# Kernel tuning notes

Hardware: AMD Instinct MI355X
Metric: run time of the kernel (lower is better)

## Reference

```python
import jax, jax.numpy as jnp
import numpy as np

N = 30000   # nodes
E = 600000  # edges (avg degree 20)
H = 128     # hidden_channels
L = 4       # num_layers
G = 64      # graphs in batch


def _init(key, shape, fan_in):
    return (jax.random.normal(key, shape, jnp.float32) / np.sqrt(fan_in)).astype(jnp.float32)


def setup_inputs() -> dict:
    key = jax.random.key(0)
    ks = jax.random.split(key, 24)
    x = jax.random.normal(ks[0], (N, 1), jnp.float32)
    pos = jax.random.normal(ks[1], (N, 3), jnp.float32)
    edge_index = jax.random.randint(ks[2], (2, E), 0, N, dtype=jnp.int32).astype(jnp.int64)
    batch = jnp.sort(jax.random.randint(ks[3], (N,), 0, G, dtype=jnp.int32)).astype(jnp.int64)

    emb_w = _init(ks[4], (1, H), 1)
    emb_b = jnp.zeros((H,), jnp.float32)

    # stacked per-layer params: msg MLP (2H+1 -> H -> H), node MLP (2H -> H -> H)
    msg_w1 = _init(ks[5], (L, 2 * H + 1, H), 2 * H + 1)
    msg_b1 = jnp.zeros((L, H), jnp.float32)
    msg_w2 = _init(ks[6], (L, H, H), H)
    msg_b2 = jnp.zeros((L, H), jnp.float32)
    node_w1 = _init(ks[7], (L, 2 * H, H), 2 * H)
    node_b1 = jnp.zeros((L, H), jnp.float32)
    node_w2 = _init(ks[8], (L, H, H), H)
    node_b2 = jnp.zeros((L, H), jnp.float32)

    out_w1 = _init(ks[9], (H, 32), H)
    out_b1 = jnp.zeros((32,), jnp.float32)
    out_w2 = _init(ks[10], (32, 1), 32)
    out_b2 = jnp.zeros((1,), jnp.float32)

    return {
        "x": x, "pos": pos, "edge_index": edge_index, "batch": batch,
        "emb_w": emb_w, "emb_b": emb_b,
        "msg_w1": msg_w1, "msg_b1": msg_b1, "msg_w2": msg_w2, "msg_b2": msg_b2,
        "node_w1": node_w1, "node_b1": node_b1, "node_w2": node_w2, "node_b2": node_b2,
        "out_w1": out_w1, "out_b1": out_b1, "out_w2": out_w2, "out_b2": out_b2,
    }


def reference(x, pos, edge_index, batch,
              emb_w, emb_b,
              msg_w1, msg_b1, msg_w2, msg_b2,
              node_w1, node_b1, node_w2, node_b2,
              out_w1, out_b1, out_w2, out_b2):
    row, col = edge_index[0], edge_index[1]  # row = source j, col = target i
    # edge scalar: squared distance (computed once, reused across layers)
    dist_sq = jnp.sum((pos[row] - pos[col]) ** 2, axis=-1, keepdims=True)  # [E,1]

    h = x @ emb_w + emb_b  # [N,H]
    for l in range(L):
        x_j = h[row]   # source features
        x_i = h[col]   # target features
        m = jnp.concatenate([x_i, x_j, dist_sq], axis=-1)           # [E, 2H+1]
        m = jax.nn.silu(m @ msg_w1[l] + msg_b1[l]) @ msg_w2[l] + msg_b2[l]  # [E,H]
        aggr = jax.ops.segment_sum(m, col, num_segments=N)          # scatter-add to targets
        nh = jnp.concatenate([h, aggr], axis=-1)                    # [N, 2H]
        h = jax.nn.silu(nh @ node_w1[l] + node_b1[l]) @ node_w2[l] + node_b2[l]
        # dropout omitted for deterministic reference (eval mode)

    g = jax.ops.segment_sum(h, batch, num_segments=G)               # global_add_pool [G,H]
    return jax.nn.silu(g @ out_w1 + out_b1) @ out_w2 + out_b2       # [G,1]
```

## Files before the change

### kernel.cpp

```cpp
#include <hip/hip_runtime.h>

typedef unsigned short u16;
typedef __bf16 bf16x8 __attribute__((ext_vector_type(8)));
typedef float f32x4 __attribute__((ext_vector_type(4)));

#define HN 128
#define TM 64
#define ASTRIDE 136

__device__ __forceinline__ u16 f2bf(float f) {
  union { float f; unsigned u; } v; v.f = f;
  unsigned r = v.u + 0x7fffu + ((v.u >> 16) & 1u);
  return (u16)(r >> 16);
}
__device__ __forceinline__ float bf2f(u16 v) {
  union { unsigned u; float f; } x; x.u = ((unsigned)v) << 16; return x.f;
}
__device__ __forceinline__ float bflo(unsigned v) {
  union { unsigned u; float f; } x; x.u = v << 16; return x.f;
}
__device__ __forceinline__ float bfhi(unsigned v) {
  union { unsigned u; float f; } x; x.u = v & 0xffff0000u; return x.f;
}
__device__ __forceinline__ float silu_f(float x) {
  float e = __builtin_amdgcn_exp2f(-1.442695041f * x);
  return x * __builtin_amdgcn_rcpf(1.f + e);
}

__global__ void pack_weights(const float* __restrict__ msg_w1, const float* __restrict__ msg_w2,
                             const float* __restrict__ node_w1, const float* __restrict__ node_w2,
                             u16* __restrict__ pw, int* __restrict__ deg,
                             float* __restrict__ g, int N_, int GH) {
  int id = blockIdx.x * 256 + threadIdx.x;
  if (id < N_) deg[id] = 0;
  if (id < GH) g[id] = 0.f;
  if (id >= 4 * 6 * 16384) return;
  int l = id / (6 * 16384);
  int rem = id % (6 * 16384);
  int m = rem / 16384;
  int e = rem % 16384;
  int kg = e >> 10;
  int n = (e >> 3) & 127;
  int j = e & 7;
  int k = kg * 8 + j;
  float v = 0.f;
  switch (m) {
    case 0: v = msg_w1[(l * 257 + k) * 128 + n]; break;
    case 1: v = msg_w1[(l * 257 + 128 + k) * 128 + n]; break;
    case 2: v = msg_w2[(l * 128 + k) * 128 + n]; break;
    case 3: v = node_w1[(l * 256 + k) * 128 + n]; break;
    case 4: v = node_w1[(l * 256 + 128 + k) * 128 + n]; break;
    case 5: v = node_w2[(l * 128 + k) * 128 + n]; break;
  }
  pw[id] = f2bf(v);
}

__device__ __forceinline__ void gemm64(const u16* s_A, const u16* s_W,
                                       int w, int quad, int m16, f32x4 acc[8]) {
#pragma unroll
  for (int ks = 0; ks < 4; ks++) {
    bf16x8 a = *(const bf16x8*)&s_A[(w * 16 + m16) * ASTRIDE + ks * 32 + quad * 8];
#pragma unroll
    for (int ct = 0; ct < 8; ct++) {
      bf16x8 b = *(const bf16x8*)&s_W[(ks * 4 + quad) * 1024 + (ct * 16 + m16) * 8];
      acc[ct] = __builtin_amdgcn_mfma_f32_16x16x32_bf16(a, b, acc[ct], 0, 0, 0);
    }
  }
}

__device__ __forceinline__ void gemm64_gb(const u16* s_A, const u16* __restrict__ gW,
                                          int w, int quad, int m16, f32x4 acc[8]) {
#pragma unroll
  for (int ks = 0; ks < 4; ks++) {
    bf16x8 a = *(const bf16x8*)&s_A[(w * 16 + m16) * ASTRIDE + ks * 32 + quad * 8];
#pragma unroll
    for (int ct = 0; ct < 8; ct++) {
      bf16x8 b = *(const bf16x8*)&gW[(ks * 4 + quad) * 1024 + (ct * 16 + m16) * 8];
      acc[ct] = __builtin_amdgcn_mfma_f32_16x16x32_bf16(a, b, acc[ct], 0, 0, 0);
    }
  }
}

__device__ __forceinline__ void gemm64_ra_gb(const bf16x8 aH[4], const u16* __restrict__ gW,
                                             int quad, int m16, f32x4 acc[8]) {
#pragma unroll
  for (int ks = 0; ks < 4; ks++) {
#pragma unroll
    for (int ct = 0; ct < 8; ct++) {
      bf16x8 b = *(const bf16x8*)&gW[(ks * 4 + quad) * 1024 + (ct * 16 + m16) * 8];
      acc[ct] = __builtin_amdgcn_mfma_f32_16x16x32_bf16(aH[ks], b, acc[ct], 0, 0, 0);
    }
  }
}

__global__ __launch_bounds__(256) void fold_kernel(
    const float* __restrict__ msg_w2, const float* __restrict__ node_w1,
    const float* __restrict__ msg_b2, const u16* __restrict__ pw,
    u16* __restrict__ pwc, float* __restrict__ vc) {
  __shared__ __align__(16) u16 s_A[TM * ASTRIDE];
  __shared__ __align__(16) u16 s_W[16384];
  const int t = threadIdx.x;
  const int w = t >> 6, lane = t & 63, quad = lane >> 4, m16 = lane & 15;
  const int b = blockIdx.x, l = b >> 1, half = b & 1;
  const int tile0 = half * 64;

  {
    int r = t >> 2, qo = (t & 3) * 32;
    const float4* src = (const float4*)(msg_w2 + (size_t)(l * 128 + tile0 + r) * 128 + qo);
    u16* dst = s_A + r * ASTRIDE + qo;
#pragma unroll
    for (int i = 0; i < 8; i++) {
      float4 v = src[i];
      ushort4 o;
      o.x = f2bf(v.x); o.y = f2bf(v.y); o.z = f2bf(v.z); o.w = f2bf(v.w);
      *(ushort4*)(dst + i * 4) = o;
    }
  }
  {
    const int4* src = (const int4*)(pw + (size_t)(l * 6 + 4) * 16384);
    int4* dst = (int4*)s_W;
#pragma unroll
    for (int i = 0; i < 8; i++) dst[t + i * 256] = src[t + i * 256];
  }
  __syncthreads();
  f32x4 acc[8];
#pragma unroll
  for (int ct = 0; ct < 8; ct++) acc[ct] = {0.f, 0.f, 0.f, 0.f};
  gemm64(s_A, s_W, w, quad, m16, acc);
#pragma unroll
  for (int ct = 0; ct < 8; ct++)
#pragma unroll
    for (int j = 0; j < 4; j++) {
      int k = tile0 + w * 16 + quad * 4 + j;
      int n = ct * 16 + m16;
      pwc[(size_t)l * 16384 + (k >> 3) * 1024 + n * 8 + (k & 7)] = f2bf(acc[ct][j]);
    }
  if (half == 0 && t < 128) {
    float s = 0.f;
    for (int np = 0; np < 128; np++)
      s += msg_b2[l * 128 + np] * node_w1[(size_t)(l * 256 + 128 + np) * 128 + t];
    vc[l * 128 + t] = s;
  }
}

__global__ void hist_kernel(const int* __restrict__ eidx, int* __restrict__ deg,
                            int* __restrict__ rnk, int E_) {
  int e = blockIdx.x * 256 + threadIdx.x;
  if (e < E_) rnk[e] = atomicAdd(&deg[eidx[E_ + e]], 1);
}

__global__ void scan1_kernel(const int* __restrict__ deg, int* __restrict__ off,
                             int* __restrict__ bsum, int n) {
  __shared__ int s[256];
  int t = threadIdx.x;
  int i = blockIdx.x * 256 + t;
  int v = (i < n) ? deg[i] : 0;
  s[t] = v;
  for (int d = 1; d < 256; d <<= 1) {
    __syncthreads();
    int x = (t >= d) ? s[t - d] : 0;
    __syncthreads();
    s[t] += x;
  }
  __syncthreads();
  if (i < n) off[i] = s[t] - v;
  if (t == 255) bsum[blockIdx.x] = s[255];
}

__global__ void scan2_kernel(int* __restrict__ bsum, int nb) {
  __shared__ int s[256];
  int t = threadIdx.x;
  int v = (t < nb) ? bsum[t] : 0;
  s[t] = v;
  for (int d = 1; d < 256; d <<= 1) {
    __syncthreads();
    int x = (t >= d) ? s[t - d] : 0;
    __syncthreads();
    s[t] += x;
  }
  __syncthreads();
  if (t < nb) bsum[t] = s[t] - v;
}

__global__ void scan3_kernel(int* __restrict__ off, const int* __restrict__ bsum, int n) {
  int i = blockIdx.x * 256 + threadIdx.x;
  if (i < n) off[i] += bsum[blockIdx.x];
}

__global__ void scatter_kernel(const int* __restrict__ eidx, const float* __restrict__ pos,
                               const int* __restrict__ off, const int* __restrict__ rnk,
                               int2* __restrict__ es8, int E_) {
  int e = blockIdx.x * 256 + threadIdx.x;
  if (e >= E_) return;
  int sr = eidx[e], tg = eidx[E_ + e];
  float dx = pos[sr * 3 + 0] - pos[tg * 3 + 0];
  float dy = pos[sr * 3 + 1] - pos[tg * 3 + 1];
  float dz = pos[sr * 3 + 2] - pos[tg * 3 + 2];
  float d = dx * dx + dy * dy + dz * dz;
  int p = off[tg] + rnk[e];
  int2 v;
  v.x = sr | (tg << 15);
  v.y = __float_as_int(d);
  es8[p] = v;
}

__global__ __launch_bounds__(256) void proj_kernel(
    const float* __restrict__ x, const float* __restrict__ emb_w,
    const float* __restrict__ emb_b, u16* __restrict__ hbf,
    u16* __restrict__ Pout, u16* __restrict__ Qout,
    const u16* __restrict__ pw, const float* __restrict__ b1, int nnodes) {
  const int t = threadIdx.x;
  const int w = t >> 6, lane = t & 63, quad = lane >> 4, m16 = lane & 15;
  const int tile0 = blockIdx.x * TM;

  int nodem = tile0 + w * 16 + m16;
  bool live = nodem < nnodes;
  if (!live) nodem = nnodes - 1;
  float xv = x[nodem];
  bf16x8 aH[4];
#pragma unroll
  for (int ks = 0; ks < 4; ks++) {
    u16 hv[8];
#pragma unroll
    for (int i = 0; i < 8; i++) {
      int c = ks * 32 + quad * 8 + i;
      hv[i] = f2bf(xv * emb_w[c] + emb_b[c]);
    }
    aH[ks] = *(bf16x8*)hv;
    if (live) *(int4*)&hbf[(size_t)nodem * HN + ks * 32 + quad * 8] = *(int4*)hv;
  }
  float bb[8];
#pragma unroll
  for (int ct = 0; ct < 8; ct++) bb[ct] = b1[ct * 16 + m16];

  f32x4 acc[8];
#pragma unroll
  for (int ct = 0; ct < 8; ct++) acc[ct] = {0.f, 0.f, 0.f, 0.f};
  gemm64_ra_gb(aH, pw, quad, m16, acc);
#pragma unroll
  for (int ct = 0; ct < 8; ct++)
#pragma unroll
    for (int j = 0; j < 4; j++) {
      int n = tile0 + w * 16 + quad * 4 + j;
      if (n < nnodes) Pout[(size_t)n * HN + ct * 16 + m16] = f2bf(acc[ct][j] + bb[ct]);
    }
#pragma unroll
  for (int ct = 0; ct < 8; ct++) acc[ct] = {0.f, 0.f, 0.f, 0.f};
  gemm64_ra_gb(aH, pw + 16384, quad, m16, acc);
#pragma unroll
  for (int ct = 0; ct < 8; ct++)
#pragma unroll
    for (int j = 0; j < 4; j++) {
      int n = tile0 + w * 16 + quad * 4 + j;
      if (n < nnodes) Qout[(size_t)n * HN + ct * 16 + m16] = f2bf(acc[ct][j]);
    }
}

__device__ __forceinline__ void edge_step_lds(
    int tg_s, float dd_s, unsigned qv,
    int& cur_s, float& p0, float& p1, float& s0, float& s1,
    const u16* __restrict__ P, float* s_S, int cp,
    float wd0, float wd1, int tile0) {
  if (tg_s != cur_s) {
    if (cur_s >= 0) {
      float* dst = &s_S[(cur_s - tile0) * HN + cp];
      atomicAdd(dst, s0);
      atomicAdd(dst + 1, s1);
    }
    cur_s = tg_s; s0 = 0.f; s1 = 0.f;
    int cg = tg_s < 0 ? 0 : tg_s;
    unsigned pv = *(const unsigned*)&P[(size_t)cg * HN + cp];
    p0 = bflo(pv); p1 = bfhi(pv);
  }
  float x0 = p0 + bflo(qv) + dd_s * wd0;
  float x1 = p1 + bfhi(qv) + dd_s * wd1;
  s0 += silu_f(x0);
  s1 += silu_f(x1);
}

template <bool FUSE>
__global__ __launch_bounds__(256) void layer_kernel(
    const u16* __restrict__ P, const u16* __restrict__ Q,
    const u16* __restrict__ hbf, u16* __restrict__ hout,
    const int* __restrict__ off, const int* __restrict__ deg,
    const float* __restrict__ w1d, const int2* __restrict__ es8,
    const u16* __restrict__ pwc, const float* __restrict__ vc,
    const u16* __restrict__ pwn, const float* __restrict__ b1, const float* __restrict__ b2,
    const u16* __restrict__ pw_next, const float* __restrict__ b1_next,
    u16* __restrict__ Pout, u16* __restrict__ Qout, int nnodes, int E_) {
  __shared__ float s_S[TM * HN];
  __shared__ __align__(16) u16 s_A[TM * ASTRIDE];
  const int t = threadIdx.x;
  const int w = t >> 6, lane = t & 63, quad = lane >> 4, m16 = lane & 15;
  const int tile0 = blockIdx.x * TM;
  u16* band = s_A + (w * 16) * ASTRIDE;

  {
    float4 z = {0.f, 0.f, 0.f, 0.f};
    float4* p4 = (float4*)s_S;
#pragma unroll
    for (int i = 0; i < 8; i++) p4[t + i * 256] = z;
  }
  __syncthreads();

  const int cp = lane * 2;
  const float2 wdv = *(const float2*)&w1d[cp];
  const float wd0 = wdv.x, wd1 = wdv.y;
  const int e_lo = off[tile0];
  const int e_hi = (tile0 + TM < nnodes) ? off[tile0 + TM] : E_;
  const int span = e_hi - e_lo;
  const int wstart = e_lo + (span * w) / 4;
  const int wend = e_lo + (span * (w + 1)) / 4;
  const int total = wend - wstart;
  const int nchunks = (total + 63) >> 6;

  int cur_s = -1;
  float s0 = 0.f, s1 = 0.f, p0 = 0.f, p1 = 0.f;

  if (nchunks > 0) {
    int2* ebuf = (int2*)band;
    {
      int e = wstart + lane;
      int2 v;
      if (e < wend) v = es8[e];
      else { v.x = (int)0xFFFF8000; v.y = 0; }
      ebuf[lane] = v;
    }
    asm volatile("s_waitcnt lgkmcnt(0)" ::: "memory");
    int tg[8]; float dd[8]; unsigned qv[8];
#pragma unroll
    for (int j = 0; j < 8; j++) {
      int2 v = ebuf[j];
      tg[j] = v.x >> 15; dd[j] = __int_as_float(v.y);
      qv[j] = *(const unsigned*)&Q[(size_t)(v.x & 0x7fff) * HN + cp];
    }

    for (int ci = 0; ci < nchunks; ci++) {
      const int2* cb = ebuf + (ci & 1) * 64;
      const int2* nb = ebuf + ((ci + 1) & 1) * 64;
      int2 vnext; vnext.x = (int)0xFFFF8000; vnext.y = 0;
      {
        int e = wstart + (ci + 1) * 64 + lane;
        if (ci + 1 < nchunks && e < wend) vnext = es8[e];
      }
#pragma unroll
      for (int g = 0; g < 7; g++) {
        int tgn[8]; float ddn[8]; unsigned qvn[8];
#pragma unroll
        for (int j = 0; j < 8; j++) {
          int2 v = cb[(g + 1) * 8 + j];
          tgn[j] = v.x >> 15; ddn[j] = __int_as_float(v.y);
          qvn[j] = *(const unsigned*)&Q[(size_t)(v.x & 0x7fff) * HN + cp];
        }
#pragma unroll
        for (int j = 0; j < 8; j++) {
          int tg_s = __builtin_amdgcn_readfirstlane(tg[j]);
          edge_step_lds(tg_s, dd[j], qv[j], cur_s, p0, p1, s0, s1, P, s_S, cp, wd0, wd1, tile0);
        }
#pragma unroll
        for (int j = 0; j < 8; j++) { tg[j] = tgn[j]; dd[j] = ddn[j]; qv[j] = qvn[j]; }
      }
      ebuf[((ci + 1) & 1) * 64 + lane] = vnext;
      asm volatile("s_waitcnt lgkmcnt(0)" ::: "memory");
      {
        int tgn[8]; float ddn[8]; unsigned qvn[8];
#pragma unroll
        for (int j = 0; j < 8; j++) {
          int2 v = nb[j];
          tgn[j] = v.x >> 15; ddn[j] = __int_as_float(v.y);
          qvn[j] = *(const unsigned*)&Q[(size_t)(v.x & 0x7fff) * HN + cp];
        }
#pragma unroll
        for (int j = 0; j < 8; j++) {
          int tg_s = __builtin_amdgcn_readfirstlane(tg[j]);
          edge_step_lds(tg_s, dd[j], qv[j], cur_s, p0, p1, s0, s1, P, s_S, cp, wd0, wd1, tile0);
        }
#pragma unroll
        for (int j = 0; j < 8; j++) { tg[j] = tgn[j]; dd[j] = ddn[j]; qv[j] = qvn[j]; }
      }
    }
    if (cur_s >= 0) {
      float* dst = &s_S[(cur_s - tile0) * HN + cp];
      atomicAdd(dst, s0);
      atomicAdd(dst + 1, s1);
    }
  }
  __syncthreads();

  const int rb = lane >> 2;
  const int qo = (lane & 3) * 32;
  int nodem = tile0 + w * 16 + m16;
  if (nodem >= nnodes) nodem = nnodes - 1;

  float bb1[8], vcr[8], bb2[8], bbn[8];
#pragma unroll
  for (int ct = 0; ct < 8; ct++) {
    bb1[ct] = b1[ct * 16 + m16];
    vcr[ct] = vc[ct * 16 + m16];
    bb2[ct] = b2[ct * 16 + m16];
    bbn[ct] = FUSE ? b1_next[ct * 16 + m16] : 0.f;
  }

  {
    const float4* src = (const float4*)&s_S[(w * 16 + rb) * HN + qo];
    u16* dst = band + rb * ASTRIDE + qo;
#pragma unroll
    for (int i = 0; i < 8; i++) {
      float4 v = src[i];
      ushort4 o;
      o.x = f2bf(v.x); o.y = f2bf(v.y); o.z = f2bf(v.z); o.w = f2bf(v.w);
      *(ushort4*)(dst + i * 4) = o;
    }
  }
  asm volatile("s_waitcnt lgkmcnt(0)" ::: "memory");
  __builtin_amdgcn_sched_barrier(0);

  f32x4 acc[8];
#pragma unroll
  for (int ct = 0; ct < 8; ct++) acc[ct] = {0.f, 0.f, 0.f, 0.f};
  gemm64_gb(s_A, pwc, w, quad, m16, acc);

  bf16x8 aH[4];
#pragma unroll
  for (int ks = 0; ks < 4; ks++)
    aH[ks] = *(const bf16x8*)&hbf[(size_t)nodem * HN + ks * 32 + quad * 8];
  gemm64_ra_gb(aH, pwn, quad, m16, acc);

  {
    float degv[4];
#pragma unroll
    for (int j = 0; j < 4; j++) {
      int n = tile0 + w * 16 + quad * 4 + j;
      if (n >= nnodes) n = nnodes - 1;
      degv[j] = (float)deg[n];
    }
#pragma unroll
    for (int ct = 0; ct < 8; ct++)
#pragma unroll
      for (int j = 0; j < 4; j++) {
        int row = quad * 4 + j;
        float xv = acc[ct][j] + bb1[ct] + degv[j] * vcr[ct];
        band[row * ASTRIDE + ct * 16 + m16] = f2bf(silu_f(xv));
      }
  }
  asm volatile("s_waitcnt lgkmcnt(0)" ::: "memory");
  __builtin_amdgcn_sched_barrier(0);

#pragma unroll
  for (int ct = 0; ct < 8; ct++) acc[ct] = {0.f, 0.f, 0.f, 0.f};
  gemm64_gb(s_A, pwn + 32768, w, quad, m16, acc);

#pragma unroll
  for (int ct = 0; ct < 8; ct++)
#pragma unroll
    for (int j = 0; j < 4; j++) {
      int row = quad * 4 + j;
      int n = tile0 + w * 16 + row;
      u16 hv = f2bf(acc[ct][j] + bb2[ct]);
      if (n < nnodes) hout[(size_t)n * HN + ct * 16 + m16] = hv;
      if (FUSE) band[row * ASTRIDE + ct * 16 + m16] = hv;
    }

  if (FUSE) {
    asm volatile("s_waitcnt lgkmcnt(0)" ::: "memory");
    __builtin_amdgcn_sched_barrier(0);
#pragma unroll
    for (int ct = 0; ct < 8; ct++) acc[ct] = {0.f, 0.f, 0.f, 0.f};
    gemm64_gb(s_A, pw_next, w, quad, m16, acc);
#pragma unroll
    for (int ct = 0; ct < 8; ct++)
#pragma unroll
      for (int j = 0; j < 4; j++) {
        int n = tile0 + w * 16 + quad * 4 + j;
        if (n < nnodes) Pout[(size_t)n * HN + ct * 16 + m16] = f2bf(acc[ct][j] + bbn[ct]);
      }
#pragma unroll
    for (int ct = 0; ct < 8; ct++) acc[ct] = {0.f, 0.f, 0.f, 0.f};
    gemm64_gb(s_A, pw_next + 16384, w, quad, m16, acc);
#pragma unroll
    for (int ct = 0; ct < 8; ct++)
#pragma unroll
      for (int j = 0; j < 4; j++) {
        int n = tile0 + w * 16 + quad * 4 + j;
        if (n < nnodes) Qout[(size_t)n * HN + ct * 16 + m16] = f2bf(acc[ct][j]);
      }
  }
}

__global__ __launch_bounds__(256) void pool_kernel(
    const u16* __restrict__ h, const int* __restrict__ batch,
    float* __restrict__ g, int N) {
  __shared__ int s_b[64];
  const int t = threadIdx.x;
  const int n0 = blockIdx.x * 64;
  if (t < 64) {
    int n = n0 + t;
    s_b[t] = (n < N) ? batch[n] : -1;
  }
  __syncthreads();
  const int cp = (t & 63) * 2;
  const int rg = t >> 6;
  int cur = -1;
  float s0 = 0.f, s1 = 0.f;
#pragma unroll 4
  for (int i = 0; i < 16; i++) {
    int r = rg * 16 + i;
    int b = s_b[r];
    if (b < 0) break;
    if (b != cur) {
      if (cur >= 0) {
        atomicAdd(&g[cur * HN + cp], s0);
        atomicAdd(&g[cur * HN + cp + 1], s1);
      }
      cur = b; s0 = 0.f; s1 = 0.f;
    }
    unsigned v = *(const unsigned*)&h[(size_t)(n0 + r) * HN + cp];
    s0 += bf2f((u16)(v & 0xffffu));
    s1 += bf2f((u16)(v >> 16));
  }
  if (cur >= 0) {
    atomicAdd(&g[cur * HN + cp], s0);
    atomicAdd(&g[cur * HN + cp + 1], s1);
  }
}

__global__ __launch_bounds__(64) void out_kernel(
    const float* __restrict__ g, const float* __restrict__ w1,
    const float* __restrict__ b1, const float* __restrict__ w2,
    const float* __restrict__ b2, float* __restrict__ out) {
  const int gi = blockIdx.x;
  const int t = threadIdx.x;
  const int c = t & 31, kh = t >> 5;
  float s = 0.f;
  for (int k = kh * 64; k < kh * 64 + 64; k++)
    s += g[gi * HN + k] * w1[k * 32 + c];
  s += __shfl_down(s, 32);
  float r = 0.f;
  if (kh == 0) r = silu_f(s + b1[c]) * w2[c];
  r += __shfl_down(r, 16);
  r += __shfl_down(r, 8);
  r += __shfl_down(r, 4);
  r += __shfl_down(r, 2);
  r += __shfl_down(r, 1);
  if (t == 0) out[gi] = r + b2[0];
}

extern "C" void kernel_launch(void* const* d_in, const int* in_sizes, int n_in,
                              void* d_out, int out_size, void* d_ws, size_t ws_size,
                              hipStream_t stream) {
  const float* x = (const float*)d_in[0];
  const float* pos = (const float*)d_in[1];
  const int* eidx = (const int*)d_in[2];
  const int* batch = (const int*)d_in[3];
  const float* emb_w = (const float*)d_in[4];
  const float* emb_b = (const float*)d_in[5];
  const float* msg_w1 = (const float*)d_in[6];
  const float* msg_b1 = (const float*)d_in[7];
  const float* msg_w2 = (const float*)d_in[8];
  const float* msg_b2 = (const float*)d_in[9];
  const float* node_w1 = (const float*)d_in[10];
  const float* node_b1 = (const float*)d_in[11];
  const float* node_w2 = (const float*)d_in[12];
  const float* node_b2 = (const float*)d_in[13];
  const float* out_w1 = (const float*)d_in[14];
  const float* out_b1 = (const float*)d_in[15];
  const float* out_w2 = (const float*)d_in[16];
  const float* out_b2 = (const float*)d_in[17];
  float* outp = (float*)d_out;

  const int N = 30000, E = 600000, G = 64;
  const size_t NH = (size_t)N * HN;

  u16* hA = (u16*)d_ws;
  u16* hB = hA + NH;
  u16* Pa = hB + NH;
  u16* Qa = Pa + NH;
  u16* Pb = Qa + NH;
  u16* Qb = Pb + NH;
  int2* es8 = (int2*)(Qb + NH);
  int* deg = (int*)(es8 + E);
  int* off = deg + N;
  int* bsum = off + N;
  float* g = (float*)(bsum + 128);
  u16* pw = (u16*)(g + G * HN);
  u16* pwc = pw + (size_t)4 * 6 * 16384;
  float* vcb = (float*)(pwc + (size_t)4 * 16384);
  int* rnk = (int*)Pb;

  const int NB = (N + 255) / 256;
  const int NTB = (N + TM - 1) / TM;

  pack_weights<<<(4 * 6 * 16384 + 255) / 256, 256, 0, stream>>>(
      msg_w1, msg_w2, node_w1, node_w2, pw, deg, g, N, G * HN);
  fold_kernel<<<8, 256, 0, stream>>>(msg_w2, node_w1, msg_b2, pw, pwc, vcb);

  hist_kernel<<<(E + 255) / 256, 256, 0, stream>>>(eidx, deg, rnk, E);
  scan1_kernel<<<NB, 256, 0, stream>>>(deg, off, bsum, N);
  scan2_kernel<<<1, 256, 0, stream>>>(bsum, NB);
  scan3_kernel<<<NB, 256, 0, stream>>>(off, bsum, N);
  scatter_kernel<<<(E + 255) / 256, 256, 0, stream>>>(eidx, pos, off, rnk, es8, E);

  proj_kernel<<<NTB, 256, 0, stream>>>(x, emb_w, emb_b, hA, Pa, Qa, pw, msg_b1, N);

  u16* hcur = hA;
  u16* hnext = hB;
  u16* Pin = Pa; u16* Qin = Qa;
  u16* Pot = Pb; u16* Qot = Qb;
  for (int l = 0; l < 4; l++) {
    const u16* pwl = pw + (size_t)(l * 6) * 16384;
    const float* w1d = msg_w1 + (size_t)(l * 257 + 256) * 128;
    if (l < 3) {
      const u16* pw_next = pw + (size_t)((l + 1) * 6) * 16384;
      layer_kernel<true><<<NTB, 256, 0, stream>>>(
          Pin, Qin, hcur, hnext, off, deg, w1d, es8,
          pwc + (size_t)l * 16384, vcb + l * 128,
          pwl + 3 * 16384, node_b1 + l * 128, node_b2 + l * 128,
          pw_next, msg_b1 + (l + 1) * 128, Pot, Qot, N, E);
    } else {
      layer_kernel<false><<<NTB, 256, 0, stream>>>(
          Pin, Qin, hcur, hnext, off, deg, w1d, es8,
          pwc + (size_t)l * 16384, vcb + l * 128,
          pwl + 3 * 16384, node_b1 + l * 128, node_b2 + l * 128,
          nullptr, nullptr, nullptr, nullptr, N, E);
    }
    u16* tmp = hcur; hcur = hnext; hnext = tmp;
    tmp = Pin; Pin = Pot; Pot = tmp;
    tmp = Qin; Qin = Qot; Qot = tmp;
  }

  pool_kernel<<<(N + 63) / 64, 256, 0, stream>>>(hcur, batch, g, N);
  out_kernel<<<G, 64, 0, stream>>>(g, out_w1, out_b1, out_w2, out_b2, outp);
}
```

Baseline: 435.2 us.

## Halve layer node tile to 32 rows and stage projection weights in LDS

Result: faster. 399.4 us (-8.2%).

```diff
diff --git a/kernel.cpp b/kernel.cpp
--- a/kernel.cpp
+++ b/kernel.cpp
@@ -6,6 +6,7 @@
 
 #define HN 128
 #define TM 64
+#define LTM 32
 #define ASTRIDE 136
 
 __device__ __forceinline__ u16 f2bf(float f) {
@@ -68,26 +69,26 @@
   }
 }
 
-__device__ __forceinline__ void gemm64_gb(const u16* s_A, const u16* __restrict__ gW,
-                                          int w, int quad, int m16, f32x4 acc[8]) {
+__device__ __forceinline__ void gemm32_gb(const u16* s_A, const u16* __restrict__ gW,
+                                          int rh, int ch, int quad, int m16, f32x4 acc[4]) {
 #pragma unroll
   for (int ks = 0; ks < 4; ks++) {
-    bf16x8 a = *(const bf16x8*)&s_A[(w * 16 + m16) * ASTRIDE + ks * 32 + quad * 8];
-#pragma unroll
-    for (int ct = 0; ct < 8; ct++) {
-      bf16x8 b = *(const bf16x8*)&gW[(ks * 4 + quad) * 1024 + (ct * 16 + m16) * 8];
+    bf16x8 a = *(const bf16x8*)&s_A[(rh * 16 + m16) * ASTRIDE + ks * 32 + quad * 8];
+#pragma unroll
+    for (int ct = 0; ct < 4; ct++) {
+      bf16x8 b = *(const bf16x8*)&gW[(ks * 4 + quad) * 1024 + ((ch * 4 + ct) * 16 + m16) * 8];
       acc[ct] = __builtin_amdgcn_mfma_f32_16x16x32_bf16(a, b, acc[ct], 0, 0, 0);
     }
   }
 }
 
-__device__ __forceinline__ void gemm64_ra_gb(const bf16x8 aH[4], const u16* __restrict__ gW,
-                                             int quad, int m16, f32x4 acc[8]) {
+__device__ __forceinline__ void gemm32_ra_gb(const bf16x8 aH[4], const u16* __restrict__ gW,
+                                             int ch, int quad, int m16, f32x4 acc[4]) {
 #pragma unroll
   for (int ks = 0; ks < 4; ks++) {
 #pragma unroll
-    for (int ct = 0; ct < 8; ct++) {
-      bf16x8 b = *(const bf16x8*)&gW[(ks * 4 + quad) * 1024 + (ct * 16 + m16) * 8];
+    for (int ct = 0; ct < 4; ct++) {
+      bf16x8 b = *(const bf16x8*)&gW[(ks * 4 + quad) * 1024 + ((ch * 4 + ct) * 16 + m16) * 8];
       acc[ct] = __builtin_amdgcn_mfma_f32_16x16x32_bf16(aH[ks], b, acc[ct], 0, 0, 0);
     }
   }
@@ -209,34 +210,47 @@
     const float* __restrict__ emb_b, u16* __restrict__ hbf,
     u16* __restrict__ Pout, u16* __restrict__ Qout,
     const u16* __restrict__ pw, const float* __restrict__ b1, int nnodes) {
+  __shared__ __align__(16) u16 s_A[TM * ASTRIDE];
+  __shared__ __align__(16) u16 s_W[16384];
   const int t = threadIdx.x;
   const int w = t >> 6, lane = t & 63, quad = lane >> 4, m16 = lane & 15;
   const int tile0 = blockIdx.x * TM;
-
-  int nodem = tile0 + w * 16 + m16;
-  bool live = nodem < nnodes;
-  if (!live) nodem = nnodes - 1;
-  float xv = x[nodem];
-  bf16x8 aH[4];
-#pragma unroll
-  for (int ks = 0; ks < 4; ks++) {
-    u16 hv[8];
-#pragma unroll
-    for (int i = 0; i < 8; i++) {
-      int c = ks * 32 + quad * 8 + i;
-      hv[i] = f2bf(xv * emb_w[c] + emb_b[c]);
-    }
-    aH[ks] = *(bf16x8*)hv;
-    if (live) *(int4*)&hbf[(size_t)nodem * HN + ks * 32 + quad * 8] = *(int4*)hv;
+  {
+    int r = t >> 2, qo = (t & 3) * 32;
+    int node = tile0 + r;
+    if (node >= nnodes) node = nnodes - 1;
+    float xv = x[node];
+    u16 hv[32];
+#pragma unroll
+    for (int i = 0; i < 32; i++) hv[i] = f2bf(xv * emb_w[qo + i] + emb_b[qo + i]);
+    u16* dst = s_A + r * ASTRIDE + qo;
+#pragma unroll
+    for (int i = 0; i < 4; i++) *(int4*)(dst + i * 8) = *(int4*)(hv + i * 8);
+    u16* gd = hbf + (size_t)node * HN + qo;
+#pragma unroll
+    for (int i = 0; i < 4; i++) *(int4*)(gd + i * 8) = *(int4*)(hv + i * 8);
+  }
+  {
+    const int4* src = (const int4*)pw;
+    int4* dst = (int4*)s_W;
+#pragma unroll
+    for (int i = 0; i < 8; i++) dst[t + i * 256] = src[t + i * 256];
+  }
+  __syncthreads();
+  f32x4 acc[8];
+#pragma unroll
+  for (int ct = 0; ct < 8; ct++) acc[ct] = {0.f, 0.f, 0.f, 0.f};
+  gemm64(s_A, s_W, w, quad, m16, acc);
+  __syncthreads();
+  {
+    const int4* src = (const int4*)(pw + 16384);
+    int4* dst = (int4*)s_W;
+#pragma unroll
+    for (int i = 0; i < 8; i++) dst[t + i * 256] = src[t + i * 256];
   }
   float bb[8];
 #pragma unroll
   for (int ct = 0; ct < 8; ct++) bb[ct] = b1[ct * 16 + m16];
-
-  f32x4 acc[8];
-#pragma unroll
-  for (int ct = 0; ct < 8; ct++) acc[ct] = {0.f, 0.f, 0.f, 0.f};
-  gemm64_ra_gb(aH, pw, quad, m16, acc);
 #pragma unroll
   for (int ct = 0; ct < 8; ct++)
 #pragma unroll
@@ -244,9 +258,10 @@
       int n = tile0 + w * 16 + quad * 4 + j;
       if (n < nnodes) Pout[(size_t)n * HN + ct * 16 + m16] = f2bf(acc[ct][j] + bb[ct]);
     }
+  __syncthreads();
 #pragma unroll
   for (int ct = 0; ct < 8; ct++) acc[ct] = {0.f, 0.f, 0.f, 0.f};
-  gemm64_ra_gb(aH, pw + 16384, quad, m16, acc);
+  gemm64(s_A, s_W, w, quad, m16, acc);
 #pragma unroll
   for (int ct = 0; ct < 8; ct++)
 #pragma unroll
@@ -288,18 +303,19 @@
     const u16* __restrict__ pwn, const float* __restrict__ b1, const float* __restrict__ b2,
     const u16* __restrict__ pw_next, const float* __restrict__ b1_next,
     u16* __restrict__ Pout, u16* __restrict__ Qout, int nnodes, int E_) {
-  __shared__ float s_S[TM * HN];
-  __shared__ __align__(16) u16 s_A[TM * ASTRIDE];
+  __shared__ float s_S[LTM * HN];
+  __shared__ __align__(16) u16 s_A[LTM * ASTRIDE];
   const int t = threadIdx.x;
   const int w = t >> 6, lane = t & 63, quad = lane >> 4, m16 = lane & 15;
-  const int tile0 = blockIdx.x * TM;
-  u16* band = s_A + (w * 16) * ASTRIDE;
+  const int tile0 = blockIdx.x * LTM;
+  const int rh = w >> 1;
+  const int ch = w & 1;
 
   {
     float4 z = {0.f, 0.f, 0.f, 0.f};
     float4* p4 = (float4*)s_S;
 #pragma unroll
-    for (int i = 0; i < 8; i++) p4[t + i * 256] = z;
+    for (int i = 0; i < 4; i++) p4[t + i * 256] = z;
   }
   __syncthreads();
 
@@ -307,7 +323,7 @@
   const float2 wdv = *(const float2*)&w1d[cp];
   const float wd0 = wdv.x, wd1 = wdv.y;
   const int e_lo = off[tile0];
-  const int e_hi = (tile0 + TM < nnodes) ? off[tile0 + TM] : E_;
+  const int e_hi = (tile0 + LTM < nnodes) ? off[tile0 + LTM] : E_;
   const int span = e_hi - e_lo;
   const int wstart = e_lo + (span * w) / 4;
   const int wend = e_lo + (span * (w + 1)) / 4;
@@ -318,7 +334,7 @@
   float s0 = 0.f, s1 = 0.f, p0 = 0.f, p1 = 0.f;
 
   if (nchunks > 0) {
-    int2* ebuf = (int2*)band;
+    int2* ebuf = (int2*)(s_A + (w * 8) * ASTRIDE);
     {
       int e = wstart + lane;
       int2 v;
@@ -387,102 +403,99 @@
   }
   __syncthreads();
 
-  const int rb = lane >> 2;
-  const int qo = (lane & 3) * 32;
-  int nodem = tile0 + w * 16 + m16;
-  if (nodem >= nnodes) nodem = nnodes - 1;
-
-  float bb1[8], vcr[8], bb2[8], bbn[8];
-#pragma unroll
-  for (int ct = 0; ct < 8; ct++) {
-    bb1[ct] = b1[ct * 16 + m16];
-    vcr[ct] = vc[ct * 16 + m16];
-    bb2[ct] = b2[ct * 16 + m16];
-    bbn[ct] = FUSE ? b1_next[ct * 16 + m16] : 0.f;
-  }
-
-  {
-    const float4* src = (const float4*)&s_S[(w * 16 + rb) * HN + qo];
-    u16* dst = band + rb * ASTRIDE + qo;
-#pragma unroll
-    for (int i = 0; i < 8; i++) {
+  {
+    int srow = w * 8 + (lane >> 3);
+    int scol = (lane & 7) * 16;
+    const float4* src = (const float4*)&s_S[srow * HN + scol];
+    u16* dst = s_A + srow * ASTRIDE + scol;
+#pragma unroll
+    for (int i = 0; i < 4; i++) {
       float4 v = src[i];
       ushort4 o;
       o.x = f2bf(v.x); o.y = f2bf(v.y); o.z = f2bf(v.z); o.w = f2bf(v.w);
       *(ushort4*)(dst + i * 4) = o;
     }
   }
-  asm volatile("s_waitcnt lgkmcnt(0)" ::: "memory");
-  __builtin_amdgcn_sched_barrier(0);
-
-  f32x4 acc[8];
-#pragma unroll
-  for (int ct = 0; ct < 8; ct++) acc[ct] = {0.f, 0.f, 0.f, 0.f};
-  gemm64_gb(s_A, pwc, w, quad, m16, acc);
+  __syncthreads();
+
+  float bb1[4], vcr[4], bb2[4], bbn[4];
+#pragma unroll
+  for (int ct = 0; ct < 4; ct++) {
+    int c = (ch * 4 + ct) * 16 + m16;
+    bb1[ct] = b1[c];
+    vcr[ct] = vc[c];
+    bb2[ct] = b2[c];
+    bbn[ct] = FUSE ? b1_next[c] : 0.f;
+  }
+  int nodem = tile0 + rh * 16 + m16;
+  if (nodem >= nnodes) nodem = nnodes - 1;
+
+  f32x4 acc[4];
+#pragma unroll
+  for (int ct = 0; ct < 4; ct++) acc[ct] = {0.f, 0.f, 0.f, 0.f};
+  gemm32_gb(s_A, pwc, rh, ch, quad, m16, acc);
 
   bf16x8 aH[4];
 #pragma unroll
   for (int ks = 0; ks < 4; ks++)
     aH[ks] = *(const bf16x8*)&hbf[(size_t)nodem * HN + ks * 32 + quad * 8];
-  gemm64_ra_gb(aH, pwn, quad, m16, acc);
+  gemm32_ra_gb(aH, pwn, ch, quad, m16, acc);
 
   {
     float degv[4];
 #pragma unroll
     for (int j = 0; j < 4; j++) {
-      int n = tile0 + w * 16 + quad * 4 + j;
+      int n = tile0 + rh * 16 + quad * 4 + j;
       if (n >= nnodes) n = nnodes - 1;
       degv[j] = (float)deg[n];
     }
 #pragma unroll
-    for (int ct = 0; ct < 8; ct++)
+    for (int ct = 0; ct < 4; ct++)
 #pragma unroll
       for (int j = 0; j < 4; j++) {
-        int row = quad * 4 + j;
+        int row = rh * 16 + quad * 4 + j;
         float xv = acc[ct][j] + bb1[ct] + degv[j] * vcr[ct];
-        band[row * ASTRIDE + ct * 16 + m16] = f2bf(silu_f(xv));
+        s_A[row * ASTRIDE + (ch * 4 + ct) * 16 + m16] = f2bf(silu_f(xv));
       }
   }
-  asm volatile("s_waitcnt lgkmcnt(0)" ::: "memory");
-  __builtin_amdgcn_sched_barrier(0);
-
-#pragma unroll
-  for (int ct = 0; ct < 8; ct++) acc[ct] = {0.f, 0.f, 0.f, 0.f};
-  gemm64_gb(s_A, pwn + 32768, w, quad, m16, acc);
-
-#pragma unroll
-  for (int ct = 0; ct < 8; ct++)
+  __syncthreads();
+
+#pragma unroll
+  for (int ct = 0; ct < 4; ct++) acc[ct] = {0.f, 0.f, 0.f, 0.f};
+  gemm32_gb(s_A, pwn + 32768, rh, ch, quad, m16, acc);
+
+#pragma unroll
+  for (int ct = 0; ct < 4; ct++)
 #pragma unroll
     for (int j = 0; j < 4; j++) {
-      int row = quad * 4 + j;
-      int n = tile0 + w * 16 + row;
+      int row = rh * 16 + quad * 4 + j;
+      int n = tile0 + row;
       u16 hv = f2bf(acc[ct][j] + bb2[ct]);
-      if (n < nnodes) hout[(size_t)n * HN + ct * 16 + m16] = hv;
-      if (FUSE) band[row * ASTRIDE + ct * 16 + m16] = hv;
+      if (n < nnodes) hout[(size_t)n * HN + (ch * 4 + ct) * 16 + m16] = hv;
+      if (FUSE) s_A[row * ASTRIDE + (ch * 4 + ct) * 16 + m16] = hv;
     }
 
   if (FUSE) {
-    asm volatile("s_waitcnt lgkmcnt(0)" ::: "memory");
-    __builtin_amdgcn_sched_barrier(0);
-#pragma unroll
-    for (int ct = 0; ct < 8; ct++) acc[ct] = {0.f, 0.f, 0.f, 0.f};
-    gemm64_gb(s_A, pw_next, w, quad, m16, acc);
-#pragma unroll
-    for (int ct = 0; ct < 8; ct++)
+    __syncthreads();
+#pragma unroll
+    for (int ct = 0; ct < 4; ct++) acc[ct] = {0.f, 0.f, 0.f, 0.f};
+    gemm32_gb(s_A, pw_next, rh, ch, quad, m16, acc);
+#pragma unroll
+    for (int ct = 0; ct < 4; ct++)
 #pragma unroll
       for (int j = 0; j < 4; j++) {
-        int n = tile0 + w * 16 + quad * 4 + j;
-        if (n < nnodes) Pout[(size_t)n * HN + ct * 16 + m16] = f2bf(acc[ct][j] + bbn[ct]);
+        int n = tile0 + rh * 16 + quad * 4 + j;
+        if (n < nnodes) Pout[(size_t)n * HN + (ch * 4 + ct) * 16 + m16] = f2bf(acc[ct][j] + bbn[ct]);
       }
 #pragma unroll
-    for (int ct = 0; ct < 8; ct++) acc[ct] = {0.f, 0.f, 0.f, 0.f};
-    gemm64_gb(s_A, pw_next + 16384, w, quad, m16, acc);
-#pragma unroll
-    for (int ct = 0; ct < 8; ct++)
+    for (int ct = 0; ct < 4; ct++) acc[ct] = {0.f, 0.f, 0.f, 0.f};
+    gemm32_gb(s_A, pw_next + 16384, rh, ch, quad, m16, acc);
+#pragma unroll
+    for (int ct = 0; ct < 4; ct++)
 #pragma unroll
       for (int j = 0; j < 4; j++) {
-        int n = tile0 + w * 16 + quad * 4 + j;
-        if (n < nnodes) Qout[(size_t)n * HN + ct * 16 + m16] = f2bf(acc[ct][j]);
+        int n = tile0 + rh * 16 + quad * 4 + j;
+        if (n < nnodes) Qout[(size_t)n * HN + (ch * 4 + ct) * 16 + m16] = f2bf(acc[ct][j]);
       }
   }
 }
@@ -589,6 +602,7 @@
 
   const int NB = (N + 255) / 256;
   const int NTB = (N + TM - 1) / TM;
+  const int NLB = (N + LTM - 1) / LTM;
 
   pack_weights<<<(4 * 6 * 16384 + 255) / 256, 256, 0, stream>>>(
       msg_w1, msg_w2, node_w1, node_w2, pw, deg, g, N, G * HN);
@@ -611,13 +625,13 @@
     const float* w1d = msg_w1 + (size_t)(l * 257 + 256) * 128;
     if (l < 3) {
       const u16* pw_next = pw + (size_t)((l + 1) * 6) * 16384;
-      layer_kernel<true><<<NTB, 256, 0, stream>>>(
+      layer_kernel<true><<<NLB, 256, 0, stream>>>(
           Pin, Qin, hcur, hnext, off, deg, w1d, es8,
           pwc + (size_t)l * 16384, vcb + l * 128,
           pwl + 3 * 16384, node_b1 + l * 128, node_b2 + l * 128,
           pw_next, msg_b1 + (l + 1) * 128, Pot, Qot, N, E);
     } else {
-      layer_kernel<false><<<NTB, 256, 0, stream>>>(
+      layer_kernel<false><<<NLB, 256, 0, stream>>>(
           Pin, Qin, hcur, hnext, off, deg, w1d, es8,
           pwc + (size_t)l * 16384, vcb + l * 128,
           pwl + 3 * 16384, node_b1 + l * 128, node_b2 + l * 128,
```
